# Kernel tuning notes

Measured on AMD Instinct MI355X. Metric: run time of the kernel, lower is better.

Reference implementation:

```python
import jax, jax.numpy as jnp
import numpy as np

N_SRC = 100000
N_TGT = 100000
N_EDGES = 1600000
D = 128
HID = 128
OUT = 64
NUM_LAYERS = 2
P_DROP = 0.1
NEG_SLOPE = 0.01


def setup_inputs() -> dict:
    key = jax.random.key(0)
    ks = jax.random.split(key, 16)
    s = 1.0 / np.sqrt(D)
    inp = {
        "x_source": jax.random.normal(ks[0], (N_SRC, D), jnp.float32),
        "x_target": jax.random.normal(ks[1], (N_TGT, D), jnp.float32),
        "Wl_tgt": jax.random.normal(ks[2], (NUM_LAYERS, D, HID), jnp.float32) * s,
        "bl_tgt": jax.random.normal(ks[3], (NUM_LAYERS, HID), jnp.float32) * s,
        "Wr_tgt": jax.random.normal(ks[4], (NUM_LAYERS, D, HID), jnp.float32) * s,
        "Wl_src": jax.random.normal(ks[5], (NUM_LAYERS, D, HID), jnp.float32) * s,
        "bl_src": jax.random.normal(ks[6], (NUM_LAYERS, HID), jnp.float32) * s,
        "Wr_src": jax.random.normal(ks[7], (NUM_LAYERS, D, HID), jnp.float32) * s,
        "W_out": jax.random.normal(ks[8], (HID, OUT), jnp.float32) * (1.0 / np.sqrt(HID)),
        "b_out": jax.random.normal(ks[9], (OUT,), jnp.float32) * 0.01,
        "edge_src": jax.random.randint(ks[10], (N_EDGES,), 0, N_SRC, jnp.int32),
        "edge_dst": jax.random.randint(ks[11], (N_EDGES,), 0, N_TGT, jnp.int32),
        "rev_src": jax.random.randint(ks[12], (N_EDGES,), 0, N_TGT, jnp.int32),
        "rev_dst": jax.random.randint(ks[13], (N_EDGES,), 0, N_SRC, jnp.int32),
    }
    return inp


def _sage(x_src, x_dst, src_idx, dst_idx, n_dst, Wl, bl, Wr):
    # mean-aggregate neighbor messages per destination node (PyG SAGEConv default)
    msg = x_src[src_idx]  # [E, D] gather
    agg = jax.ops.segment_sum(msg, dst_idx, num_segments=n_dst)  # [n_dst, D]
    cnt = jax.ops.segment_sum(jnp.ones((src_idx.shape[0],), msg.dtype), dst_idx,
                              num_segments=n_dst)
    mean = agg / jnp.maximum(cnt, 1.0)[:, None]
    return mean @ Wl + bl + x_dst @ Wr


def _dropout(x, key):
    keep = jax.random.bernoulli(key, 1.0 - P_DROP, x.shape)
    return jnp.where(keep, x / (1.0 - P_DROP), jnp.zeros((), x.dtype))


def reference(x_source, x_target, Wl_tgt, bl_tgt, Wr_tgt, Wl_src, bl_src, Wr_src,
              W_out, b_out, edge_src, edge_dst, rev_src, rev_dst):
    dkey = jax.random.key(42)
    xs, xt = x_source, x_target
    for l in range(NUM_LAYERS):
        # ('source','edge','target'): target receives from source
        new_t = _sage(xs, xt, edge_src, edge_dst, N_TGT, Wl_tgt[l], bl_tgt[l], Wr_tgt[l])
        # ('target','rev_edge','source'): source receives from target
        new_s = _sage(xt, xs, rev_src, rev_dst, N_SRC, Wl_src[l], bl_src[l], Wr_src[l])
        new_t = jax.nn.leaky_relu(new_t, NEG_SLOPE)
        new_s = jax.nn.leaky_relu(new_s, NEG_SLOPE)
        new_t = _dropout(new_t, jax.random.fold_in(dkey, 2 * l))
        new_s = _dropout(new_s, jax.random.fold_in(dkey, 2 * l + 1))
        xs, xt = new_s, new_t
    return xs @ W_out + b_out
```

## Files before the change

### kernel.cpp

```cpp
#include <hip/hip_runtime.h>
#include <stdint.h>

#define NN 100000
#define NE 1600000
#define DD 128
#define HB 1024
#define G8 12544
#define SUBN 98
#define NSUB 128
#define NND 100352
#define K2 16
#define RCAP 2304

typedef unsigned short u16;
typedef short short8 __attribute__((ext_vector_type(8)));
typedef float floatx4 __attribute__((ext_vector_type(4)));
typedef int intx4 __attribute__((ext_vector_type(4)));

__device__ static inline u16 f2bf(float f){
  unsigned u = __float_as_uint(f);
  unsigned r = u + 0x7FFFu + ((u >> 16) & 1u);
  return (u16)(r >> 16);
}

__host__ __device__ static inline unsigned rotl32(unsigned x, int r){
  return (x << r) | (x >> (32 - r));
}

__host__ __device__ static inline void tf2x32(unsigned k0, unsigned k1,
                                              unsigned c0, unsigned c1,
                                              unsigned &o0, unsigned &o1)
{
  const unsigned ks2 = k0 ^ k1 ^ 0x1BD11BDAu;
  unsigned x0 = c0 + k0, x1 = c1 + k1;
#define TFR(r) { x0 += x1; x1 = rotl32(x1, (r)); x1 ^= x0; }
  TFR(13) TFR(15) TFR(26) TFR(6)   x0 += k1;  x1 += ks2 + 1u;
  TFR(17) TFR(29) TFR(16) TFR(24)  x0 += ks2; x1 += k0 + 2u;
  TFR(13) TFR(15) TFR(26) TFR(6)   x0 += k0;  x1 += k1 + 3u;
  TFR(17) TFR(29) TFR(16) TFR(24)  x0 += k1;  x1 += ks2 + 4u;
  TFR(13) TFR(15) TFR(26) TFR(6)   x0 += ks2; x1 += k0 + 5u;
#undef TFR
  o0 = x0; o1 = x1;
}

__device__ static inline float drop_scale(unsigned k0, unsigned k1, unsigned j)
{
  unsigned o0, o1;
  tf2x32(k0, k1, 0u, j, o0, o1);
  const unsigned bits = o0 ^ o1;
  const float u = __uint_as_float((bits >> 9) | 0x3F800000u) - 1.0f;
  return (u < 0.9f) ? (1.0f / 0.9f) : 0.0f;
}

__global__ __launch_bounds__(256) void k_hist(const int* __restrict__ e_dst,
                                              const int* __restrict__ r_dst,
                                              int* __restrict__ hist){
  __shared__ int h[16];
  const int t = threadIdx.x;
  if (t < 16) h[t] = 0;
  __syncthreads();
  const int QT = 2 * (NE / 4);
  for (int i = blockIdx.x * 256 + t; i < QT; i += HB * 256){
    int dir = (i >= NE / 4);
    int qi = dir ? i - NE / 4 : i;
    const int* dp = dir ? r_dst : e_dst;
    intx4 d = __builtin_nontemporal_load((const intx4*)dp + qi);
    int bb = dir << 3;
    atomicAdd(&h[bb + d.x / G8], 1);
    atomicAdd(&h[bb + d.y / G8], 1);
    atomicAdd(&h[bb + d.z / G8], 1);
    atomicAdd(&h[bb + d.w / G8], 1);
  }
  __syncthreads();
  if (t < 16) hist[t * HB + blockIdx.x] = h[t];
}

__global__ __launch_bounds__(256) void k_scanA(int* __restrict__ hist){
  __shared__ int sh[16 * HB];
  __shared__ int tot[256];
  const int t = threadIdx.x;
  const int N = 16 * HB;
  for (int k = t; k < N; k += 256) sh[k] = hist[k];
  __syncthreads();
  int s = 0;
  #pragma unroll 4
  for (int k = 0; k < 64; ++k)
    s += sh[(t >> 4) * HB + (t & 15) + (k << 4)];
  tot[t] = s;
  __syncthreads();
  int v = s;
  for (int off = 1; off < 256; off <<= 1){
    int u = (t >= off) ? tot[t - off] : 0;
    __syncthreads();
    tot[t] += u;
    __syncthreads();
  }
  int run = tot[t] - v;
  for (int k = 0; k < 64; ++k){
    int idx = (t >> 4) * HB + (t & 15) + (k << 4);
    int xv = sh[idx];
    sh[idx] = run;
    run += xv;
  }
  __syncthreads();
  for (int k = t; k < N; k += 256) hist[k] = sh[k];
  if (t == 255) hist[N] = tot[255];
}

__global__ __launch_bounds__(256) void k_scatter1(const int* __restrict__ e_src,
                                                  const int* __restrict__ e_dst,
                                                  const int* __restrict__ r_src,
                                                  const int* __restrict__ r_dst,
                                                  const int* __restrict__ base,
                                                  unsigned* __restrict__ stage){
  __shared__ int cur[16];
  const int t = threadIdx.x;
  if (t < 16) cur[t] = base[t * HB + blockIdx.x];
  __syncthreads();
  const int QT = 2 * (NE / 4);
  for (int i = blockIdx.x * 256 + t; i < QT; i += HB * 256){
    int dir = (i >= NE / 4);
    int qi = dir ? i - NE / 4 : i;
    const int* dp = dir ? r_dst : e_dst;
    const int* sp = dir ? r_src : e_src;
    intx4 d = __builtin_nontemporal_load((const intx4*)dp + qi);
    intx4 sv = __builtin_nontemporal_load((const intx4*)sp + qi);
    int bb = dir << 3;
    int g, p;
    g = d.x / G8; p = atomicAdd(&cur[bb + g], 1);
    stage[p] = (unsigned)sv.x | ((unsigned)(d.x - g * G8) << 17);
    g = d.y / G8; p = atomicAdd(&cur[bb + g], 1);
    stage[p] = (unsigned)sv.y | ((unsigned)(d.y - g * G8) << 17);
    g = d.z / G8; p = atomicAdd(&cur[bb + g], 1);
    stage[p] = (unsigned)sv.z | ((unsigned)(d.z - g * G8) << 17);
    g = d.w / G8; p = atomicAdd(&cur[bb + g], 1);
    stage[p] = (unsigned)sv.w | ((unsigned)(d.w - g * G8) << 17);
  }
}

__global__ __launch_bounds__(256) void k_hist2(const unsigned* __restrict__ stage,
                                               const int* __restrict__ base,
                                               int* __restrict__ hist2){
  __shared__ int h2[NSUB];
  const int b16 = blockIdx.x / K2, k = blockIdx.x % K2;
  const int t = threadIdx.x;
  if (t < NSUB) h2[t] = 0;
  __syncthreads();
  const int beg = base[b16 * HB];
  const int end = base[(b16 + 1) * HB];
  for (int i = beg + k * 256 + t; i < end; i += K2 * 256){
    unsigned p = stage[i];
    atomicAdd(&h2[(int)(p >> 17) / SUBN], 1);
  }
  __syncthreads();
  if (t < NSUB) hist2[(b16 * NSUB + t) * K2 + k] = h2[t];
}

__global__ __launch_bounds__(256) void k_scanB(int* __restrict__ hist2){
  __shared__ int sh[16 * NSUB * K2];
  __shared__ int tot[256];
  const int t = threadIdx.x;
  const int N = 16 * NSUB * K2;
  for (int k = t; k < N; k += 256) sh[k] = hist2[k];
  __syncthreads();
  int s = 0;
  for (int j = 0; j < 128; ++j) s += sh[t * 128 + j];
  tot[t] = s;
  __syncthreads();
  int v = s;
  for (int off = 1; off < 256; off <<= 1){
    int u = (t >= off) ? tot[t - off] : 0;
    __syncthreads();
    tot[t] += u;
    __syncthreads();
  }
  int run = tot[t] - v;
  for (int j = 0; j < 128; ++j){
    int xv = sh[t * 128 + j];
    sh[t * 128 + j] = run;
    run += xv;
  }
  __syncthreads();
  for (int k = t; k < N; k += 256) hist2[k] = sh[k];
}

__global__ __launch_bounds__(256) void k_scatter2(const unsigned* __restrict__ stage,
                                                  const int* __restrict__ base,
                                                  const int* __restrict__ h2s,
                                                  unsigned* __restrict__ stage2){
  __shared__ int cur[NSUB];
  const int b16 = blockIdx.x / K2, k = blockIdx.x % K2;
  const int t = threadIdx.x;
  if (t < NSUB) cur[t] = h2s[(b16 * NSUB + t) * K2 + k];
  __syncthreads();
  const int beg = base[b16 * HB];
  const int end = base[(b16 + 1) * HB];
  for (int i = beg + k * 256 + t; i < end; i += K2 * 256){
    unsigned p = stage[i];
    int pos = atomicAdd(&cur[(int)(p >> 17) / SUBN], 1);
    stage2[pos] = p;
  }
}

__global__ __launch_bounds__(256) void k_fill4(const unsigned* __restrict__ stage2,
                                               const int* __restrict__ h2s,
                                               int* __restrict__ ptr,
                                               int* __restrict__ csr){
  __shared__ unsigned rec[RCAP];
  __shared__ unsigned srt[RCAP];
  __shared__ int ldeg[SUBN], lptr[SUBN], lcur[SUBN];
  const int sb = blockIdx.x;
  const int b16 = sb >> 7, sub = sb & 127;
  const int dir = b16 >> 3, g = b16 & 7;
  const int t = threadIdx.x;
  const int beg = h2s[sb * K2];
  const int end = (sb == 2047) ? 2 * NE : h2s[(sb + 1) * K2];
  int n = end - beg;
  if (n > RCAP) n = RCAP;
  for (int i = t; i < n; i += 256) rec[i] = stage2[beg + i];
  if (t < SUBN) ldeg[t] = 0;
  __syncthreads();
  const int nl0 = sub * SUBN;
  for (int i = t; i < n; i += 256)
    atomicAdd(&ldeg[(int)(rec[i] >> 17) - nl0], 1);
  __syncthreads();
  if (t == 0){
    int run = 0;
    for (int s = 0; s < SUBN; ++s){ lptr[s] = run; lcur[s] = run; run += ldeg[s]; }
  }
  __syncthreads();
  for (int i = t; i < n; i += 256){
    int rl = (int)(rec[i] >> 17) - nl0;
    int pos = atomicAdd(&lcur[rl], 1);
    srt[pos] = rec[i] & 0x1FFFFu;
  }
  __syncthreads();
  const int node0 = g * G8 + nl0;
  if (t < SUBN) ptr[dir * NND + node0 + t] = beg + lptr[t];
  if (sb == 2047 && t == 0) ptr[2 * NND] = 2 * NE;
  for (int i = t; i < n; i += 256) csr[beg + i] = (int)srt[i];
}

__global__ __launch_bounds__(256) void k_cvt2(const float* __restrict__ ina,
                                              const float* __restrict__ inb,
                                              u16* __restrict__ oa,
                                              u16* __restrict__ ob, int n8){
  int i = blockIdx.x * 256 + threadIdx.x;
  const float* in = ina; u16* out = oa;
  if (i >= n8){ i -= n8; in = inb; out = ob; }
  floatx4 a = __builtin_nontemporal_load((const floatx4*)in + (size_t)i * 2);
  floatx4 b = __builtin_nontemporal_load((const floatx4*)in + (size_t)i * 2 + 1);
  u16 v[8] = { f2bf(a[0]), f2bf(a[1]), f2bf(a[2]), f2bf(a[3]),
               f2bf(b[0]), f2bf(b[1]), f2bf(b[2]), f2bf(b[3]) };
  *(uint4*)(out + (size_t)i * 8) = *(const uint4*)v;
}

__global__ __launch_bounds__(256) void k_prep(const float* __restrict__ Wl_tgt,
    const float* __restrict__ Wr_tgt, const float* __restrict__ Wl_src,
    const float* __restrict__ Wr_src, const float* __restrict__ Wo,
    u16* __restrict__ Wsw0, u16* __restrict__ Wsw1, u16* __restrict__ Wsw2,
    u16* __restrict__ Wswo){
  int b = blockIdx.x;
  if (b < 48){
    const float *Wl, *Wr; u16* dst;
    if (b < 16){ Wl = Wl_tgt; Wr = Wr_tgt; dst = Wsw0; }
    else if (b < 32){ Wl = Wl_src; Wr = Wr_src; dst = Wsw1; b -= 16; }
    else { Wl = Wl_src + 16384; Wr = Wr_src + 16384; dst = Wsw2; b -= 32; }
    int idx = b * 256 + threadIdx.x;
    int lane = idx & 63, tile = idx >> 6;
    int kt = tile >> 3, nt = tile & 7;
    int n = nt * 16 + (lane & 15);
    int kb = kt * 32 + (lane >> 4) * 8;
    u16 v[8];
    #pragma unroll
    for (int j = 0; j < 8; ++j){
      int k = kb + j;
      float w = (k < 128) ? Wl[(size_t)k * 128 + n] : Wr[(size_t)(k - 128) * 128 + n];
      v[j] = f2bf(w);
    }
    *(uint4*)(dst + (size_t)idx * 8) = *(const uint4*)v;
  } else {
    int idx = (b - 48) * 256 + threadIdx.x;
    int lane = idx & 63, tile = idx >> 6;
    int kt = tile >> 2, nt = tile & 3;
    int n = nt * 16 + (lane & 15);
    int kb = kt * 32 + (lane >> 4) * 8;
    u16 v[8];
    #pragma unroll
    for (int j = 0; j < 8; ++j)
      v[j] = f2bf(Wo[(size_t)(kb + j) * 64 + n]);
    *(uint4*)(Wswo + (size_t)idx * 8) = *(const uint4*)v;
  }
}

__device__ static inline void agg_body(const u16* __restrict__ x,
                                       const int* __restrict__ pd,
                                       const int* __restrict__ csr,
                                       u16* __restrict__ out, int blk){
  const int row = blk * 4 + (threadIdx.x >> 6);
  const int lane = threadIdx.x & 63;
  const int sub = lane >> 4, l4 = lane & 15;
  const int beg = pd[row], end = pd[row + 1];
  const int cnt = end - beg;
  float a[8] = {0.f,0.f,0.f,0.f,0.f,0.f,0.f,0.f};
  int e = 0;
  for (; e + 7 < cnt; e += 8){
    int s0 = csr[beg + e + sub];
    int s1 = csr[beg + e + 4 + sub];
    uint4 v0 = *(const uint4*)(x + (size_t)s0 * DD + l4 * 8);
    uint4 v1 = *(const uint4*)(x + (size_t)s1 * DD + l4 * 8);
    a[0] += __uint_as_float(v0.x << 16); a[1] += __uint_as_float(v0.x & 0xFFFF0000u);
    a[2] += __uint_as_float(v0.y << 16); a[3] += __uint_as_float(v0.y & 0xFFFF0000u);
    a[4] += __uint_as_float(v0.z << 16); a[5] += __uint_as_float(v0.z & 0xFFFF0000u);
    a[6] += __uint_as_float(v0.w << 16); a[7] += __uint_as_float(v0.w & 0xFFFF0000u);
    a[0] += __uint_as_float(v1.x << 16); a[1] += __uint_as_float(v1.x & 0xFFFF0000u);
    a[2] += __uint_as_float(v1.y << 16); a[3] += __uint_as_float(v1.y & 0xFFFF0000u);
    a[4] += __uint_as_float(v1.z << 16); a[5] += __uint_as_float(v1.z & 0xFFFF0000u);
    a[6] += __uint_as_float(v1.w << 16); a[7] += __uint_as_float(v1.w & 0xFFFF0000u);
  }
  for (; e + 3 < cnt; e += 4){
    int s0 = csr[beg + e + sub];
    uint4 v0 = *(const uint4*)(x + (size_t)s0 * DD + l4 * 8);
    a[0] += __uint_as_float(v0.x << 16); a[1] += __uint_as_float(v0.x & 0xFFFF0000u);
    a[2] += __uint_as_float(v0.y << 16); a[3] += __uint_as_float(v0.y & 0xFFFF0000u);
    a[4] += __uint_as_float(v0.z << 16); a[5] += __uint_as_float(v0.z & 0xFFFF0000u);
    a[6] += __uint_as_float(v0.w << 16); a[7] += __uint_as_float(v0.w & 0xFFFF0000u);
  }
  if (e + sub < cnt){
    int s0 = csr[beg + e + sub];
    uint4 v0 = *(const uint4*)(x + (size_t)s0 * DD + l4 * 8);
    a[0] += __uint_as_float(v0.x << 16); a[1] += __uint_as_float(v0.x & 0xFFFF0000u);
    a[2] += __uint_as_float(v0.y << 16); a[3] += __uint_as_float(v0.y & 0xFFFF0000u);
    a[4] += __uint_as_float(v0.z << 16); a[5] += __uint_as_float(v0.z & 0xFFFF0000u);
    a[6] += __uint_as_float(v0.w << 16); a[7] += __uint_as_float(v0.w & 0xFFFF0000u);
  }
  #pragma unroll
  for (int i = 0; i < 8; ++i){
    a[i] += __shfl_xor(a[i], 16);
    a[i] += __shfl_xor(a[i], 32);
  }
  const float inv = (cnt > 0) ? (1.0f / (float)cnt) : 1.0f;
  if (sub == 0){
    unsigned pk[4];
    #pragma unroll
    for (int i = 0; i < 4; ++i)
      pk[i] = (unsigned)f2bf(a[2*i] * inv) | ((unsigned)f2bf(a[2*i+1] * inv) << 16);
    *(uint4*)(out + (size_t)row * DD + l4 * 8) = make_uint4(pk[0], pk[1], pk[2], pk[3]);
  }
}

__global__ __launch_bounds__(256) void k_aggD(const u16* __restrict__ x0,
    const u16* __restrict__ x1, const int* __restrict__ ptr,
    const int* __restrict__ csr, u16* __restrict__ o0, u16* __restrict__ o1){
  int b = blockIdx.x;
  if (b < NN / 4) agg_body(x0, ptr, csr, o0, b);
  else            agg_body(x1, ptr + NND, csr, o1, b - NN / 4);
}

__global__ __launch_bounds__(256) void k_agg1(const u16* __restrict__ x,
    const int* __restrict__ ptr, const int* __restrict__ csr,
    u16* __restrict__ out){
  agg_body(x, ptr + NND, csr, out, blockIdx.x);
}

__device__ static inline void fused_body(const u16* __restrict__ Am,
    const u16* __restrict__ X, const u16* __restrict__ Wsw,
    const float* __restrict__ bias, u16* __restrict__ outH,
    unsigned key0, unsigned key1, int blk)
{
  const int wave = threadIdx.x >> 6, lane = threadIdx.x & 63;
  const int quad = lane >> 4, col0 = lane & 15;
  const int row0 = blk * 64 + wave * 16;
  int m = row0 + col0;
  if (m >= NN) m = NN - 1;

  floatx4 acc[8];
  #pragma unroll
  for (int i = 0; i < 8; ++i) acc[i] = (floatx4)0.f;

  #pragma unroll
  for (int kt = 0; kt < 8; ++kt){
    const int k = kt * 32 + quad * 8;
    const u16* ap = (k < 128) ? (Am + (size_t)m * 128 + k)
                              : (X  + (size_t)m * 128 + (k - 128));
    short8 a = __builtin_nontemporal_load((const short8*)ap);
    #pragma unroll
    for (int nt = 0; nt < 8; ++nt){
      short8 b = *(const short8*)(Wsw + (size_t)(((kt * 8 + nt) * 64 + lane) * 8));
      acc[nt] = __builtin_amdgcn_mfma_f32_16x16x32_bf16(a, b, acc[nt], 0, 0, 0);
    }
  }

  #pragma unroll
  for (int nt = 0; nt < 8; ++nt){
    const int col = nt * 16 + col0;
    const float bj = bias[col];
    #pragma unroll
    for (int rg = 0; rg < 4; ++rg){
      const int r = row0 + quad * 4 + rg;
      if (r < NN){
        float h = acc[nt][rg] + bj;
        h = (h >= 0.f) ? h : 0.01f * h;
        unsigned j = (unsigned)r * 128u + (unsigned)col;
        h *= drop_scale(key0, key1, j);
        outH[(size_t)r * 128 + col] = f2bf(h);
      }
    }
  }
}

#define GB ((NN + 63) / 64)

__global__ __launch_bounds__(256) void k_fusedD(
    const u16* __restrict__ A0, const u16* __restrict__ X0,
    const u16* __restrict__ W0, const float* __restrict__ b0,
    u16* __restrict__ o0, unsigned k00, unsigned k01,
    const u16* __restrict__ A1, const u16* __restrict__ X1,
    const u16* __restrict__ W1, const float* __restrict__ b1,
    u16* __restrict__ o1, unsigned k10, unsigned k11)
{
  int b = blockIdx.x;
  if (b < GB) fused_body(A0, X0, W0, b0, o0, k00, k01, b);
  else        fused_body(A1, X1, W1, b1, o1, k10, k11, b - GB);
}

__global__ __launch_bounds__(256) void k_fused(const u16* __restrict__ Am,
    const u16* __restrict__ X, const u16* __restrict__ Wsw,
    const float* __restrict__ bias, u16* __restrict__ outH,
    unsigned key0, unsigned key1)
{
  fused_body(Am, X, Wsw, bias, outH, key0, key1, blockIdx.x);
}

__global__ __launch_bounds__(256) void k_out(const u16* __restrict__ H,
    const u16* __restrict__ Wsw, const float* __restrict__ bias,
    float* __restrict__ out)
{
  const int wave = threadIdx.x >> 6, lane = threadIdx.x & 63;
  const int quad = lane >> 4, col0 = lane & 15;
  const int row0 = blockIdx.x * 64 + wave * 16;
  int m = row0 + col0;
  if (m >= NN) m = NN - 1;

  floatx4 acc[4];
  #pragma unroll
  for (int i = 0; i < 4; ++i) acc[i] = (floatx4)0.f;

  #pragma unroll
  for (int kt = 0; kt < 4; ++kt){
    short8 a = __builtin_nontemporal_load(
        (const short8*)(H + (size_t)m * 128 + kt * 32 + quad * 8));
    #pragma unroll
    for (int nt = 0; nt < 4; ++nt){
      short8 b = *(const short8*)(Wsw + (size_t)(((kt * 4 + nt) * 64 + lane) * 8));
      acc[nt] = __builtin_amdgcn_mfma_f32_16x16x32_bf16(a, b, acc[nt], 0, 0, 0);
    }
  }

  #pragma unroll
  for (int nt = 0; nt < 4; ++nt){
    const int col = nt * 16 + col0;
    const float bj = bias[col];
    #pragma unroll
    for (int rg = 0; rg < 4; ++rg){
      const int r = row0 + quad * 4 + rg;
      if (r < NN)
        out[(size_t)r * 64 + col] = acc[nt][rg] + bj;
    }
  }
}

extern "C" void kernel_launch(void* const* d_in, const int* in_sizes, int n_in,
                              void* d_out, int out_size, void* d_ws, size_t ws_size,
                              hipStream_t stream)
{
  const float* x_src  = (const float*)d_in[0];
  const float* x_tgt  = (const float*)d_in[1];
  const float* Wl_tgt = (const float*)d_in[2];
  const float* bl_tgt = (const float*)d_in[3];
  const float* Wr_tgt = (const float*)d_in[4];
  const float* Wl_src = (const float*)d_in[5];
  const float* bl_src = (const float*)d_in[6];
  const float* Wr_src = (const float*)d_in[7];
  const float* W_o    = (const float*)d_in[8];
  const float* b_o    = (const float*)d_in[9];
  const int*   e_src  = (const int*)d_in[10];
  const int*   e_dst  = (const int*)d_in[11];
  const int*   r_src  = (const int*)d_in[12];
  const int*   r_dst  = (const int*)d_in[13];
  float* out = (float*)d_out;
  (void)in_sizes; (void)n_in; (void)out_size; (void)ws_size;

  char* ws = (char*)d_ws;
  size_t off = 0;
  auto alloc = [&](size_t bytes) -> char* {
    char* p = ws + off; off += (bytes + 255) & ~(size_t)255; return p;
  };
  unsigned* stage1 = (unsigned*)alloc((size_t)2 * NE * 4);
  unsigned* stage2 = (unsigned*)alloc((size_t)2 * NE * 4);
  u16* A_t  = (u16*)stage1;
  u16* A_s  = (u16*)alloc((size_t)NN * DD * 2);
  u16* Xs   = (u16*)alloc((size_t)NN * DD * 2);
  u16* Xt   = (u16*)alloc((size_t)NN * DD * 2);
  u16* B    = (u16*)alloc((size_t)NN * DD * 2);
  u16* C    = (u16*)alloc((size_t)NN * DD * 2);
  u16* Wsw0 = (u16*)alloc(256 * 128 * 2);
  u16* Wsw1 = (u16*)alloc(256 * 128 * 2);
  u16* Wsw2 = (u16*)alloc(256 * 128 * 2);
  u16* Wswo = (u16*)alloc(128 * 64 * 2);
  int* csr  = (int*)alloc((size_t)2 * NE * 4);
  int* ptr  = (int*)alloc((size_t)(2 * NND + 1) * 4);
  int* hist  = (int*)alloc((size_t)(16 * HB + 1) * 4);
  int* hist2 = (int*)alloc((size_t)(16 * NSUB * K2) * 4);

  unsigned kt0a, kt0b, ks0a, ks0b, ks1a, ks1b;
  tf2x32(0u, 42u, 0u, 0u, kt0a, kt0b);
  tf2x32(0u, 42u, 0u, 1u, ks0a, ks0b);
  tf2x32(0u, 42u, 0u, 3u, ks1a, ks1b);

  const int CB = NN * DD / 8 / 256;

  k_cvt2<<<2 * CB, 256, 0, stream>>>(x_src, x_tgt, Xs, Xt, NN * DD / 8);
  k_prep<<<52, 256, 0, stream>>>(Wl_tgt, Wr_tgt, Wl_src, Wr_src, W_o,
                                 Wsw0, Wsw1, Wsw2, Wswo);

  k_hist<<<HB, 256, 0, stream>>>(e_dst, r_dst, hist);
  k_scanA<<<1, 256, 0, stream>>>(hist);
  k_scatter1<<<HB, 256, 0, stream>>>(e_src, e_dst, r_src, r_dst, hist, stage1);
  k_hist2<<<16 * K2, 256, 0, stream>>>(stage1, hist, hist2);
  k_scanB<<<1, 256, 0, stream>>>(hist2);
  k_scatter2<<<16 * K2, 256, 0, stream>>>(stage1, hist, hist2, stage2);
  k_fill4<<<2048, 256, 0, stream>>>(stage2, hist2, ptr, csr);

  const int AB = NN / 4;
  k_aggD<<<2 * AB, 256, 0, stream>>>(Xs, Xt, ptr, csr, A_t, A_s);
  k_fusedD<<<2 * GB, 256, 0, stream>>>(A_t, Xt, Wsw0, bl_tgt, B, kt0a, kt0b,
                                       A_s, Xs, Wsw1, bl_src, C, ks0a, ks0b);
  k_agg1<<<AB, 256, 0, stream>>>(B, ptr, csr, A_t);
  k_fused<<<GB, 256, 0, stream>>>(A_t, C, Wsw2, bl_src + 128, B, ks1a, ks1b);
  k_out<<<GB, 256, 0, stream>>>(B, Wswo, b_o, out);
}
```

Baseline: 576.2 us.

## Precompute dropout masks as bitmasks in aggregation kernels to hide latency

The Threefry dropout RNG moves out of the MFMA epilogue and into the memory-bound aggregation kernels. There each wave computes keep bits for its row with ballots and stores them as two 64-bit masks per row. The fused GEMM epilogue then reads these bitmasks instead of running Threefry for every output element. The aim is to hide RNG ALU work under gather latency, at the cost of small extra mask buffers and the extra traffic to write and read them.

```diff
diff --git a/kernel.cpp b/kernel.cpp
--- a/kernel.cpp
+++ b/kernel.cpp
@@ -13,6 +13,7 @@
 #define RCAP 2304
 
 typedef unsigned short u16;
+typedef unsigned long long u64;
 typedef short short8 __attribute__((ext_vector_type(8)));
 typedef float floatx4 __attribute__((ext_vector_type(4)));
 typedef int intx4 __attribute__((ext_vector_type(4)));
@@ -43,13 +44,13 @@
   o0 = x0; o1 = x1;
 }
 
-__device__ static inline float drop_scale(unsigned k0, unsigned k1, unsigned j)
+__device__ static inline int drop_keep(unsigned k0, unsigned k1, unsigned j)
 {
   unsigned o0, o1;
   tf2x32(k0, k1, 0u, j, o0, o1);
   const unsigned bits = o0 ^ o1;
   const float u = __uint_as_float((bits >> 9) | 0x3F800000u) - 1.0f;
-  return (u < 0.9f) ? (1.0f / 0.9f) : 0.0f;
+  return u < 0.9f;
 }
 
 __global__ __launch_bounds__(256) void k_hist(const int* __restrict__ e_dst,
@@ -296,7 +297,9 @@
 __device__ static inline void agg_body(const u16* __restrict__ x,
                                        const int* __restrict__ pd,
                                        const int* __restrict__ csr,
-                                       u16* __restrict__ out, int blk){
+                                       u16* __restrict__ out,
+                                       u64* __restrict__ msk,
+                                       unsigned key0, unsigned key1, int blk){
   const int row = blk * 4 + (threadIdx.x >> 6);
   const int lane = threadIdx.x & 63;
   const int sub = lane >> 4, l4 = lane & 15;
@@ -334,12 +337,15 @@
     a[4] += __uint_as_float(v0.z << 16); a[5] += __uint_as_float(v0.z & 0xFFFF0000u);
     a[6] += __uint_as_float(v0.w << 16); a[7] += __uint_as_float(v0.w & 0xFFFF0000u);
   }
+  u64 mA = __ballot(drop_keep(key0, key1, (unsigned)row * 128u + (unsigned)lane));
+  u64 mB = __ballot(drop_keep(key0, key1, (unsigned)row * 128u + 64u + (unsigned)lane));
   #pragma unroll
   for (int i = 0; i < 8; ++i){
     a[i] += __shfl_xor(a[i], 16);
     a[i] += __shfl_xor(a[i], 32);
   }
   const float inv = (cnt > 0) ? (1.0f / (float)cnt) : 1.0f;
+  if (lane < 2) msk[(size_t)row * 2 + lane] = lane ? mB : mA;
   if (sub == 0){
     unsigned pk[4];
     #pragma unroll
@@ -351,22 +357,25 @@
 
 __global__ __launch_bounds__(256) void k_aggD(const u16* __restrict__ x0,
     const u16* __restrict__ x1, const int* __restrict__ ptr,
-    const int* __restrict__ csr, u16* __restrict__ o0, u16* __restrict__ o1){
+    const int* __restrict__ csr, u16* __restrict__ o0, u16* __restrict__ o1,
+    u64* __restrict__ m0, u64* __restrict__ m1,
+    unsigned k00, unsigned k01, unsigned k10, unsigned k11){
   int b = blockIdx.x;
-  if (b < NN / 4) agg_body(x0, ptr, csr, o0, b);
-  else            agg_body(x1, ptr + NND, csr, o1, b - NN / 4);
+  if (b < NN / 4) agg_body(x0, ptr, csr, o0, m0, k00, k01, b);
+  else            agg_body(x1, ptr + NND, csr, o1, m1, k10, k11, b - NN / 4);
 }
 
 __global__ __launch_bounds__(256) void k_agg1(const u16* __restrict__ x,
     const int* __restrict__ ptr, const int* __restrict__ csr,
-    u16* __restrict__ out){
-  agg_body(x, ptr + NND, csr, out, blockIdx.x);
+    u16* __restrict__ out, u64* __restrict__ msk,
+    unsigned key0, unsigned key1){
+  agg_body(x, ptr + NND, csr, out, msk, key0, key1, blockIdx.x);
 }
 
 __device__ static inline void fused_body(const u16* __restrict__ Am,
     const u16* __restrict__ X, const u16* __restrict__ Wsw,
     const float* __restrict__ bias, u16* __restrict__ outH,
-    unsigned key0, unsigned key1, int blk)
+    const u64* __restrict__ msk, int blk)
 {
   const int wave = threadIdx.x >> 6, lane = threadIdx.x & 63;
   const int quad = lane >> 4, col0 = lane & 15;
@@ -391,18 +400,28 @@
     }
   }
 
+  u64 w0[4], w1[4];
+  #pragma unroll
+  for (int rg = 0; rg < 4; ++rg){
+    int r = row0 + quad * 4 + rg;
+    size_t rr = (size_t)((r < NN) ? r : (NN - 1)) * 2;
+    w0[rg] = msk[rr];
+    w1[rg] = msk[rr + 1];
+  }
+
   #pragma unroll
   for (int nt = 0; nt < 8; ++nt){
     const int col = nt * 16 + col0;
     const float bj = bias[col];
+    const int sh = col & 63;
     #pragma unroll
     for (int rg = 0; rg < 4; ++rg){
       const int r = row0 + quad * 4 + rg;
       if (r < NN){
         float h = acc[nt][rg] + bj;
         h = (h >= 0.f) ? h : 0.01f * h;
-        unsigned j = (unsigned)r * 128u + (unsigned)col;
-        h *= drop_scale(key0, key1, j);
+        u64 w = (nt < 4) ? w0[rg] : w1[rg];
+        h = ((w >> sh) & 1ull) ? h * (1.0f / 0.9f) : 0.0f;
         outH[(size_t)r * 128 + col] = f2bf(h);
       }
     }
@@ -414,22 +433,22 @@
 __global__ __launch_bounds__(256) void k_fusedD(
     const u16* __restrict__ A0, const u16* __restrict__ X0,
     const u16* __restrict__ W0, const float* __restrict__ b0,
-    u16* __restrict__ o0, unsigned k00, unsigned k01,
+    u16* __restrict__ o0, const u64* __restrict__ m0,
     const u16* __restrict__ A1, const u16* __restrict__ X1,
     const u16* __restrict__ W1, const float* __restrict__ b1,
-    u16* __restrict__ o1, unsigned k10, unsigned k11)
+    u16* __restrict__ o1, const u64* __restrict__ m1)
 {
   int b = blockIdx.x;
-  if (b < GB) fused_body(A0, X0, W0, b0, o0, k00, k01, b);
-  else        fused_body(A1, X1, W1, b1, o1, k10, k11, b - GB);
+  if (b < GB) fused_body(A0, X0, W0, b0, o0, m0, b);
+  else        fused_body(A1, X1, W1, b1, o1, m1, b - GB);
 }
 
 __global__ __launch_bounds__(256) void k_fused(const u16* __restrict__ Am,
     const u16* __restrict__ X, const u16* __restrict__ Wsw,
     const float* __restrict__ bias, u16* __restrict__ outH,
-    unsigned key0, unsigned key1)
-{
-  fused_body(Am, X, Wsw, bias, outH, key0, key1, blockIdx.x);
+    const u64* __restrict__ msk)
+{
+  fused_body(Am, X, Wsw, bias, outH, msk, blockIdx.x);
 }
 
 __global__ __launch_bounds__(256) void k_out(const u16* __restrict__ H,
@@ -512,6 +531,9 @@
   int* ptr  = (int*)alloc((size_t)(2 * NND + 1) * 4);
   int* hist  = (int*)alloc((size_t)(16 * HB + 1) * 4);
   int* hist2 = (int*)alloc((size_t)(16 * NSUB * K2) * 4);
+  u64* M0t  = (u64*)alloc((size_t)NN * 2 * 8);
+  u64* M0s  = (u64*)alloc((size_t)NN * 2 * 8);
+  u64* M1s  = (u64*)alloc((size_t)NN * 2 * 8);
 
   unsigned kt0a, kt0b, ks0a, ks0b, ks1a, ks1b;
   tf2x32(0u, 42u, 0u, 0u, kt0a, kt0b);
@@ -533,10 +555,11 @@
   k_fill4<<<2048, 256, 0, stream>>>(stage2, hist2, ptr, csr);
 
   const int AB = NN / 4;
-  k_aggD<<<2 * AB, 256, 0, stream>>>(Xs, Xt, ptr, csr, A_t, A_s);
-  k_fusedD<<<2 * GB, 256, 0, stream>>>(A_t, Xt, Wsw0, bl_tgt, B, kt0a, kt0b,
-                                       A_s, Xs, Wsw1, bl_src, C, ks0a, ks0b);
-  k_agg1<<<AB, 256, 0, stream>>>(B, ptr, csr, A_t);
-  k_fused<<<GB, 256, 0, stream>>>(A_t, C, Wsw2, bl_src + 128, B, ks1a, ks1b);
+  k_aggD<<<2 * AB, 256, 0, stream>>>(Xs, Xt, ptr, csr, A_t, A_s,
+                                     M0t, M0s, kt0a, kt0b, ks0a, ks0b);
+  k_fusedD<<<2 * GB, 256, 0, stream>>>(A_t, Xt, Wsw0, bl_tgt, B, M0t,
+                                       A_s, Xs, Wsw1, bl_src, C, M0s);
+  k_agg1<<<AB, 256, 0, stream>>>(B, ptr, csr, A_t, M1s, ks1a, ks1b);
+  k_fused<<<GB, 256, 0, stream>>>(A_t, C, Wsw2, bl_src + 128, B, M1s);
   k_out<<<GB, 256, 0, stream>>>(B, Wswo, b_o, out);
 }
```

Measured after the change: 568.9 us. Within noise of the previous version (-1.3%).

## Fuse neighbor aggregation into MFMA layer kernel via swizzled LDS tile

Applied to the files above, without the earlier changes.

Each layer's mean aggregation now runs inside the GEMM kernel. Every block gathers and averages 64 destination rows into a swizzled shared-memory tile, then feeds that tile straight into the MFMA loop, so the aggregated matrix no longer goes through global memory. Dropout masks are computed once per row with ballots during aggregation and stored as bitmasks, replacing per-element Threefry calls in the epilogue. The conversion, histogram and weight-prep kernels are merged into one launch, and accumulation uses paired float2 adds. In exchange, each block serialises 16 gather rows per wave, with fewer blocks in flight to hide gather latency.

```diff
diff --git a/kernel.cpp b/kernel.cpp
--- a/kernel.cpp
+++ b/kernel.cpp
@@ -13,8 +13,10 @@
 #define RCAP 2304
 
 typedef unsigned short u16;
+typedef unsigned long long u64;
 typedef short short8 __attribute__((ext_vector_type(8)));
 typedef float floatx4 __attribute__((ext_vector_type(4)));
+typedef float floatx2 __attribute__((ext_vector_type(2)));
 typedef int intx4 __attribute__((ext_vector_type(4)));
 
 __device__ static inline u16 f2bf(float f){
@@ -43,36 +45,100 @@
   o0 = x0; o1 = x1;
 }
 
-__device__ static inline float drop_scale(unsigned k0, unsigned k1, unsigned j)
+__device__ static inline int drop_keep(unsigned k0, unsigned k1, unsigned j)
 {
   unsigned o0, o1;
   tf2x32(k0, k1, 0u, j, o0, o1);
   const unsigned bits = o0 ^ o1;
   const float u = __uint_as_float((bits >> 9) | 0x3F800000u) - 1.0f;
-  return (u < 0.9f) ? (1.0f / 0.9f) : 0.0f;
-}
-
-__global__ __launch_bounds__(256) void k_hist(const int* __restrict__ e_dst,
-                                              const int* __restrict__ r_dst,
-                                              int* __restrict__ hist){
-  __shared__ int h[16];
-  const int t = threadIdx.x;
-  if (t < 16) h[t] = 0;
-  __syncthreads();
-  const int QT = 2 * (NE / 4);
-  for (int i = blockIdx.x * 256 + t; i < QT; i += HB * 256){
-    int dir = (i >= NE / 4);
-    int qi = dir ? i - NE / 4 : i;
-    const int* dp = dir ? r_dst : e_dst;
-    intx4 d = __builtin_nontemporal_load((const intx4*)dp + qi);
-    int bb = dir << 3;
-    atomicAdd(&h[bb + d.x / G8], 1);
-    atomicAdd(&h[bb + d.y / G8], 1);
-    atomicAdd(&h[bb + d.z / G8], 1);
-    atomicAdd(&h[bb + d.w / G8], 1);
-  }
-  __syncthreads();
-  if (t < 16) hist[t * HB + blockIdx.x] = h[t];
+  return u < 0.9f;
+}
+
+__device__ static inline void acc4(floatx2 &p0, floatx2 &p1, floatx2 &p2,
+                                   floatx2 &p3, uint4 v){
+  floatx2 t0, t1, t2, t3;
+  t0[0] = __uint_as_float(v.x << 16); t0[1] = __uint_as_float(v.x & 0xFFFF0000u);
+  t1[0] = __uint_as_float(v.y << 16); t1[1] = __uint_as_float(v.y & 0xFFFF0000u);
+  t2[0] = __uint_as_float(v.z << 16); t2[1] = __uint_as_float(v.z & 0xFFFF0000u);
+  t3[0] = __uint_as_float(v.w << 16); t3[1] = __uint_as_float(v.w & 0xFFFF0000u);
+  p0 += t0; p1 += t1; p2 += t2; p3 += t3;
+}
+
+#define CVB 12500
+__global__ __launch_bounds__(256) void k_pre(
+    const float* __restrict__ ina, const float* __restrict__ inb,
+    u16* __restrict__ oa, u16* __restrict__ ob, int n8,
+    const int* __restrict__ e_dst, const int* __restrict__ r_dst,
+    int* __restrict__ hist,
+    const float* __restrict__ Wl_tgt, const float* __restrict__ Wr_tgt,
+    const float* __restrict__ Wl_src, const float* __restrict__ Wr_src,
+    const float* __restrict__ Wo,
+    u16* __restrict__ Wsw0, u16* __restrict__ Wsw1, u16* __restrict__ Wsw2,
+    u16* __restrict__ Wswo)
+{
+  const int blk = blockIdx.x;
+  const int t = threadIdx.x;
+  if (blk < CVB){
+    int i = blk * 256 + t;
+    const float* in = ina; u16* out = oa;
+    if (i >= n8){ i -= n8; in = inb; out = ob; }
+    floatx4 a = __builtin_nontemporal_load((const floatx4*)in + (size_t)i * 2);
+    floatx4 c = __builtin_nontemporal_load((const floatx4*)in + (size_t)i * 2 + 1);
+    u16 v[8] = { f2bf(a[0]), f2bf(a[1]), f2bf(a[2]), f2bf(a[3]),
+                 f2bf(c[0]), f2bf(c[1]), f2bf(c[2]), f2bf(c[3]) };
+    *(uint4*)(out + (size_t)i * 8) = *(const uint4*)v;
+  } else if (blk < CVB + HB){
+    const int hb = blk - CVB;
+    __shared__ int h[16];
+    if (t < 16) h[t] = 0;
+    __syncthreads();
+    const int QT = 2 * (NE / 4);
+    for (int i = hb * 256 + t; i < QT; i += HB * 256){
+      int dir = (i >= NE / 4);
+      int qi = dir ? i - NE / 4 : i;
+      const int* dp = dir ? r_dst : e_dst;
+      intx4 d = __builtin_nontemporal_load((const intx4*)dp + qi);
+      int bb = dir << 3;
+      atomicAdd(&h[bb + d.x / G8], 1);
+      atomicAdd(&h[bb + d.y / G8], 1);
+      atomicAdd(&h[bb + d.z / G8], 1);
+      atomicAdd(&h[bb + d.w / G8], 1);
+    }
+    __syncthreads();
+    if (t < 16) hist[t * HB + hb] = h[t];
+  } else {
+    int b = blk - CVB - HB;
+    if (b < 48){
+      const float *Wl, *Wr; u16* dst;
+      if (b < 16){ Wl = Wl_tgt; Wr = Wr_tgt; dst = Wsw0; }
+      else if (b < 32){ Wl = Wl_src; Wr = Wr_src; dst = Wsw1; b -= 16; }
+      else { Wl = Wl_src + 16384; Wr = Wr_src + 16384; dst = Wsw2; b -= 32; }
+      int idx = b * 256 + t;
+      int lane = idx & 63, tile = idx >> 6;
+      int kt = tile >> 3, nt = tile & 7;
+      int n = nt * 16 + (lane & 15);
+      int kb = kt * 32 + (lane >> 4) * 8;
+      u16 v[8];
+      #pragma unroll
+      for (int j = 0; j < 8; ++j){
+        int k = kb + j;
+        float w = (k < 128) ? Wl[(size_t)k * 128 + n] : Wr[(size_t)(k - 128) * 128 + n];
+        v[j] = f2bf(w);
+      }
+      *(uint4*)(dst + (size_t)idx * 8) = *(const uint4*)v;
+    } else {
+      int idx = (b - 48) * 256 + t;
+      int lane = idx & 63, tile = idx >> 6;
+      int kt = tile >> 2, nt = tile & 3;
+      int n = nt * 16 + (lane & 15);
+      int kb = kt * 32 + (lane >> 4) * 8;
+      u16 v[8];
+      #pragma unroll
+      for (int j = 0; j < 8; ++j)
+        v[j] = f2bf(Wo[(size_t)(kb + j) * 64 + n]);
+      *(uint4*)(Wswo + (size_t)idx * 8) = *(const uint4*)v;
+    }
+  }
 }
 
 __global__ __launch_bounds__(256) void k_scanA(int* __restrict__ hist){
@@ -241,149 +307,86 @@
   for (int i = t; i < n; i += 256) csr[beg + i] = (int)srt[i];
 }
 
-__global__ __launch_bounds__(256) void k_cvt2(const float* __restrict__ ina,
-                                              const float* __restrict__ inb,
-                                              u16* __restrict__ oa,
-                                              u16* __restrict__ ob, int n8){
-  int i = blockIdx.x * 256 + threadIdx.x;
-  const float* in = ina; u16* out = oa;
-  if (i >= n8){ i -= n8; in = inb; out = ob; }
-  floatx4 a = __builtin_nontemporal_load((const floatx4*)in + (size_t)i * 2);
-  floatx4 b = __builtin_nontemporal_load((const floatx4*)in + (size_t)i * 2 + 1);
-  u16 v[8] = { f2bf(a[0]), f2bf(a[1]), f2bf(a[2]), f2bf(a[3]),
-               f2bf(b[0]), f2bf(b[1]), f2bf(b[2]), f2bf(b[3]) };
-  *(uint4*)(out + (size_t)i * 8) = *(const uint4*)v;
-}
-
-__global__ __launch_bounds__(256) void k_prep(const float* __restrict__ Wl_tgt,
-    const float* __restrict__ Wr_tgt, const float* __restrict__ Wl_src,
-    const float* __restrict__ Wr_src, const float* __restrict__ Wo,
-    u16* __restrict__ Wsw0, u16* __restrict__ Wsw1, u16* __restrict__ Wsw2,
-    u16* __restrict__ Wswo){
-  int b = blockIdx.x;
-  if (b < 48){
-    const float *Wl, *Wr; u16* dst;
-    if (b < 16){ Wl = Wl_tgt; Wr = Wr_tgt; dst = Wsw0; }
-    else if (b < 32){ Wl = Wl_src; Wr = Wr_src; dst = Wsw1; b -= 16; }
-    else { Wl = Wl_src + 16384; Wr = Wr_src + 16384; dst = Wsw2; b -= 32; }
-    int idx = b * 256 + threadIdx.x;
-    int lane = idx & 63, tile = idx >> 6;
-    int kt = tile >> 3, nt = tile & 7;
-    int n = nt * 16 + (lane & 15);
-    int kb = kt * 32 + (lane >> 4) * 8;
-    u16 v[8];
+__device__ static inline void mf_body(const u16* __restrict__ xsrc,
+    const u16* __restrict__ xdst, const int* __restrict__ pd,
+    const int* __restrict__ csr, const u16* __restrict__ Wsw,
+    const float* __restrict__ bias, u16* __restrict__ outH,
+    unsigned key0, unsigned key1, int blk)
+{
+  __shared__ u16 As[64 * DD];
+  __shared__ u64 Ms[64][2];
+  const int wave = threadIdx.x >> 6, lane = threadIdx.x & 63;
+  const int sub = lane >> 4, l4 = lane & 15;
+  const int row0 = blk * 64;
+
+  for (int i = 0; i < 16; ++i){
+    const int lr = wave * 16 + i;
+    const int row = row0 + lr;
+    int beg = 0, cnt = 0;
+    if (row < NN){ beg = pd[row]; cnt = pd[row + 1] - beg; }
+    floatx2 p0 = (floatx2)0.f, p1 = (floatx2)0.f,
+            p2 = (floatx2)0.f, p3 = (floatx2)0.f;
+    int e = 0;
+    for (; e + 7 < cnt; e += 8){
+      int s0 = csr[beg + e + sub];
+      int s1 = csr[beg + e + 4 + sub];
+      uint4 v0 = *(const uint4*)(xsrc + (size_t)s0 * DD + l4 * 8);
+      uint4 v1 = *(const uint4*)(xsrc + (size_t)s1 * DD + l4 * 8);
+      acc4(p0, p1, p2, p3, v0);
+      acc4(p0, p1, p2, p3, v1);
+    }
+    for (; e + 3 < cnt; e += 4){
+      int s0 = csr[beg + e + sub];
+      uint4 v0 = *(const uint4*)(xsrc + (size_t)s0 * DD + l4 * 8);
+      acc4(p0, p1, p2, p3, v0);
+    }
+    if (e + sub < cnt){
+      int s0 = csr[beg + e + sub];
+      uint4 v0 = *(const uint4*)(xsrc + (size_t)s0 * DD + l4 * 8);
+      acc4(p0, p1, p2, p3, v0);
+    }
+    const int rm = (row < NN) ? row : NN - 1;
+    u64 mA = __ballot(drop_keep(key0, key1, (unsigned)rm * 128u + (unsigned)lane));
+    u64 mB = __ballot(drop_keep(key0, key1, (unsigned)rm * 128u + 64u + (unsigned)lane));
+    if (lane == 0){ Ms[lr][0] = mA; Ms[lr][1] = mB; }
+    float a[8] = { p0[0], p0[1], p1[0], p1[1], p2[0], p2[1], p3[0], p3[1] };
     #pragma unroll
     for (int j = 0; j < 8; ++j){
-      int k = kb + j;
-      float w = (k < 128) ? Wl[(size_t)k * 128 + n] : Wr[(size_t)(k - 128) * 128 + n];
-      v[j] = f2bf(w);
-    }
-    *(uint4*)(dst + (size_t)idx * 8) = *(const uint4*)v;
-  } else {
-    int idx = (b - 48) * 256 + threadIdx.x;
-    int lane = idx & 63, tile = idx >> 6;
-    int kt = tile >> 2, nt = tile & 3;
-    int n = nt * 16 + (lane & 15);
-    int kb = kt * 32 + (lane >> 4) * 8;
-    u16 v[8];
-    #pragma unroll
-    for (int j = 0; j < 8; ++j)
-      v[j] = f2bf(Wo[(size_t)(kb + j) * 64 + n]);
-    *(uint4*)(Wswo + (size_t)idx * 8) = *(const uint4*)v;
-  }
-}
-
-__device__ static inline void agg_body(const u16* __restrict__ x,
-                                       const int* __restrict__ pd,
-                                       const int* __restrict__ csr,
-                                       u16* __restrict__ out, int blk){
-  const int row = blk * 4 + (threadIdx.x >> 6);
-  const int lane = threadIdx.x & 63;
-  const int sub = lane >> 4, l4 = lane & 15;
-  const int beg = pd[row], end = pd[row + 1];
-  const int cnt = end - beg;
-  float a[8] = {0.f,0.f,0.f,0.f,0.f,0.f,0.f,0.f};
-  int e = 0;
-  for (; e + 7 < cnt; e += 8){
-    int s0 = csr[beg + e + sub];
-    int s1 = csr[beg + e + 4 + sub];
-    uint4 v0 = *(const uint4*)(x + (size_t)s0 * DD + l4 * 8);
-    uint4 v1 = *(const uint4*)(x + (size_t)s1 * DD + l4 * 8);
-    a[0] += __uint_as_float(v0.x << 16); a[1] += __uint_as_float(v0.x & 0xFFFF0000u);
-    a[2] += __uint_as_float(v0.y << 16); a[3] += __uint_as_float(v0.y & 0xFFFF0000u);
-    a[4] += __uint_as_float(v0.z << 16); a[5] += __uint_as_float(v0.z & 0xFFFF0000u);
-    a[6] += __uint_as_float(v0.w << 16); a[7] += __uint_as_float(v0.w & 0xFFFF0000u);
-    a[0] += __uint_as_float(v1.x << 16); a[1] += __uint_as_float(v1.x & 0xFFFF0000u);
-    a[2] += __uint_as_float(v1.y << 16); a[3] += __uint_as_float(v1.y & 0xFFFF0000u);
-    a[4] += __uint_as_float(v1.z << 16); a[5] += __uint_as_float(v1.z & 0xFFFF0000u);
-    a[6] += __uint_as_float(v1.w << 16); a[7] += __uint_as_float(v1.w & 0xFFFF0000u);
-  }
-  for (; e + 3 < cnt; e += 4){
-    int s0 = csr[beg + e + sub];
-    uint4 v0 = *(const uint4*)(x + (size_t)s0 * DD + l4 * 8);
-    a[0] += __uint_as_float(v0.x << 16); a[1] += __uint_as_float(v0.x & 0xFFFF0000u);
-    a[2] += __uint_as_float(v0.y << 16); a[3] += __uint_as_float(v0.y & 0xFFFF0000u);
-    a[4] += __uint_as_float(v0.z << 16); a[5] += __uint_as_float(v0.z & 0xFFFF0000u);
-    a[6] += __uint_as_float(v0.w << 16); a[7] += __uint_as_float(v0.w & 0xFFFF0000u);
-  }
-  if (e + sub < cnt){
-    int s0 = csr[beg + e + sub];
-    uint4 v0 = *(const uint4*)(x + (size_t)s0 * DD + l4 * 8);
-    a[0] += __uint_as_float(v0.x << 16); a[1] += __uint_as_float(v0.x & 0xFFFF0000u);
-    a[2] += __uint_as_float(v0.y << 16); a[3] += __uint_as_float(v0.y & 0xFFFF0000u);
-    a[4] += __uint_as_float(v0.z << 16); a[5] += __uint_as_float(v0.z & 0xFFFF0000u);
-    a[6] += __uint_as_float(v0.w << 16); a[7] += __uint_as_float(v0.w & 0xFFFF0000u);
-  }
-  #pragma unroll
-  for (int i = 0; i < 8; ++i){
-    a[i] += __shfl_xor(a[i], 16);
-    a[i] += __shfl_xor(a[i], 32);
-  }
-  const float inv = (cnt > 0) ? (1.0f / (float)cnt) : 1.0f;
-  if (sub == 0){
-    unsigned pk[4];
-    #pragma unroll
-    for (int i = 0; i < 4; ++i)
-      pk[i] = (unsigned)f2bf(a[2*i] * inv) | ((unsigned)f2bf(a[2*i+1] * inv) << 16);
-    *(uint4*)(out + (size_t)row * DD + l4 * 8) = make_uint4(pk[0], pk[1], pk[2], pk[3]);
-  }
-}
-
-__global__ __launch_bounds__(256) void k_aggD(const u16* __restrict__ x0,
-    const u16* __restrict__ x1, const int* __restrict__ ptr,
-    const int* __restrict__ csr, u16* __restrict__ o0, u16* __restrict__ o1){
-  int b = blockIdx.x;
-  if (b < NN / 4) agg_body(x0, ptr, csr, o0, b);
-  else            agg_body(x1, ptr + NND, csr, o1, b - NN / 4);
-}
-
-__global__ __launch_bounds__(256) void k_agg1(const u16* __restrict__ x,
-    const int* __restrict__ ptr, const int* __restrict__ csr,
-    u16* __restrict__ out){
-  agg_body(x, ptr + NND, csr, out, blockIdx.x);
-}
-
-__device__ static inline void fused_body(const u16* __restrict__ Am,
-    const u16* __restrict__ X, const u16* __restrict__ Wsw,
-    const float* __restrict__ bias, u16* __restrict__ outH,
-    unsigned key0, unsigned key1, int blk)
-{
-  const int wave = threadIdx.x >> 6, lane = threadIdx.x & 63;
+      a[j] += __shfl_xor(a[j], 16);
+      a[j] += __shfl_xor(a[j], 32);
+    }
+    const float inv = (cnt > 0) ? (1.0f / (float)cnt) : 1.0f;
+    if (sub == 0){
+      unsigned pk[4];
+      #pragma unroll
+      for (int j = 0; j < 4; ++j)
+        pk[j] = (unsigned)f2bf(a[2*j] * inv) | ((unsigned)f2bf(a[2*j+1] * inv) << 16);
+      const int ch = l4 ^ (lr & 15);
+      *(uint4*)(As + lr * DD + ch * 8) = make_uint4(pk[0], pk[1], pk[2], pk[3]);
+    }
+  }
+  __syncthreads();
+
   const int quad = lane >> 4, col0 = lane & 15;
-  const int row0 = blk * 64 + wave * 16;
-  int m = row0 + col0;
+  const int ml = wave * 16 + col0;
+  int m = row0 + ml;
   if (m >= NN) m = NN - 1;
 
   floatx4 acc[8];
   #pragma unroll
-  for (int i = 0; i < 8; ++i) acc[i] = (floatx4)0.f;
+  for (int j = 0; j < 8; ++j) acc[j] = (floatx4)0.f;
 
   #pragma unroll
   for (int kt = 0; kt < 8; ++kt){
-    const int k = kt * 32 + quad * 8;
-    const u16* ap = (k < 128) ? (Am + (size_t)m * 128 + k)
-                              : (X  + (size_t)m * 128 + (k - 128));
-    short8 a = __builtin_nontemporal_load((const short8*)ap);
+    short8 a;
+    if (kt < 4){
+      const int k = kt * 32 + quad * 8;
+      const int ch = (k >> 3) ^ (ml & 15);
+      a = *(const short8*)(As + ml * DD + ch * 8);
+    } else {
+      const int k = (kt - 4) * 32 + quad * 8;
+      a = __builtin_nontemporal_load((const short8*)(xdst + (size_t)m * 128 + k));
+    }
     #pragma unroll
     for (int nt = 0; nt < 8; ++nt){
       short8 b = *(const short8*)(Wsw + (size_t)(((kt * 8 + nt) * 64 + lane) * 8));
@@ -395,14 +398,16 @@
   for (int nt = 0; nt < 8; ++nt){
     const int col = nt * 16 + col0;
     const float bj = bias[col];
+    const int sh = col & 63;
     #pragma unroll
     for (int rg = 0; rg < 4; ++rg){
-      const int r = row0 + quad * 4 + rg;
+      const int lr2 = wave * 16 + quad * 4 + rg;
+      const int r = row0 + lr2;
       if (r < NN){
         float h = acc[nt][rg] + bj;
         h = (h >= 0.f) ? h : 0.01f * h;
-        unsigned j = (unsigned)r * 128u + (unsigned)col;
-        h *= drop_scale(key0, key1, j);
+        u64 w = Ms[lr2][nt >> 2];
+        h = ((w >> sh) & 1ull) ? h * (1.0f / 0.9f) : 0.0f;
         outH[(size_t)r * 128 + col] = f2bf(h);
       }
     }
@@ -411,25 +416,26 @@
 
 #define GB ((NN + 63) / 64)
 
-__global__ __launch_bounds__(256) void k_fusedD(
-    const u16* __restrict__ A0, const u16* __restrict__ X0,
+__global__ __launch_bounds__(256) void k_mfD(
+    const u16* __restrict__ Xs, const u16* __restrict__ Xt,
+    const int* __restrict__ ptr, const int* __restrict__ csr,
     const u16* __restrict__ W0, const float* __restrict__ b0,
-    u16* __restrict__ o0, unsigned k00, unsigned k01,
-    const u16* __restrict__ A1, const u16* __restrict__ X1,
+    u16* __restrict__ oB, unsigned k00, unsigned k01,
     const u16* __restrict__ W1, const float* __restrict__ b1,
-    u16* __restrict__ o1, unsigned k10, unsigned k11)
+    u16* __restrict__ oC, unsigned k10, unsigned k11)
 {
   int b = blockIdx.x;
-  if (b < GB) fused_body(A0, X0, W0, b0, o0, k00, k01, b);
-  else        fused_body(A1, X1, W1, b1, o1, k10, k11, b - GB);
-}
-
-__global__ __launch_bounds__(256) void k_fused(const u16* __restrict__ Am,
-    const u16* __restrict__ X, const u16* __restrict__ Wsw,
-    const float* __restrict__ bias, u16* __restrict__ outH,
-    unsigned key0, unsigned key1)
-{
-  fused_body(Am, X, Wsw, bias, outH, key0, key1, blockIdx.x);
+  if (b < GB) mf_body(Xs, Xt, ptr,       csr, W0, b0, oB, k00, k01, b);
+  else        mf_body(Xt, Xs, ptr + NND, csr, W1, b1, oC, k10, k11, b - GB);
+}
+
+__global__ __launch_bounds__(256) void k_mf1(
+    const u16* __restrict__ Bh, const u16* __restrict__ Ch,
+    const int* __restrict__ ptr, const int* __restrict__ csr,
+    const u16* __restrict__ W2, const float* __restrict__ b2,
+    u16* __restrict__ oH, unsigned ka, unsigned kb)
+{
+  mf_body(Bh, Ch, ptr + NND, csr, W2, b2, oH, ka, kb, blockIdx.x);
 }
 
 __global__ __launch_bounds__(256) void k_out(const u16* __restrict__ H,
@@ -498,8 +504,7 @@
   };
   unsigned* stage1 = (unsigned*)alloc((size_t)2 * NE * 4);
   unsigned* stage2 = (unsigned*)alloc((size_t)2 * NE * 4);
-  u16* A_t  = (u16*)stage1;
-  u16* A_s  = (u16*)alloc((size_t)NN * DD * 2);
+  u16* H1   = (u16*)stage1;
   u16* Xs   = (u16*)alloc((size_t)NN * DD * 2);
   u16* Xt   = (u16*)alloc((size_t)NN * DD * 2);
   u16* B    = (u16*)alloc((size_t)NN * DD * 2);
@@ -518,13 +523,10 @@
   tf2x32(0u, 42u, 0u, 1u, ks0a, ks0b);
   tf2x32(0u, 42u, 0u, 3u, ks1a, ks1b);
 
-  const int CB = NN * DD / 8 / 256;
-
-  k_cvt2<<<2 * CB, 256, 0, stream>>>(x_src, x_tgt, Xs, Xt, NN * DD / 8);
-  k_prep<<<52, 256, 0, stream>>>(Wl_tgt, Wr_tgt, Wl_src, Wr_src, W_o,
-                                 Wsw0, Wsw1, Wsw2, Wswo);
-
-  k_hist<<<HB, 256, 0, stream>>>(e_dst, r_dst, hist);
+  k_pre<<<CVB + HB + 52, 256, 0, stream>>>(x_src, x_tgt, Xs, Xt, NN * DD / 8,
+                                           e_dst, r_dst, hist,
+                                           Wl_tgt, Wr_tgt, Wl_src, Wr_src, W_o,
+                                           Wsw0, Wsw1, Wsw2, Wswo);
   k_scanA<<<1, 256, 0, stream>>>(hist);
   k_scatter1<<<HB, 256, 0, stream>>>(e_src, e_dst, r_src, r_dst, hist, stage1);
   k_hist2<<<16 * K2, 256, 0, stream>>>(stage1, hist, hist2);
@@ -532,11 +534,10 @@
   k_scatter2<<<16 * K2, 256, 0, stream>>>(stage1, hist, hist2, stage2);
   k_fill4<<<2048, 256, 0, stream>>>(stage2, hist2, ptr, csr);
 
-  const int AB = NN / 4;
-  k_aggD<<<2 * AB, 256, 0, stream>>>(Xs, Xt, ptr, csr, A_t, A_s);
-  k_fusedD<<<2 * GB, 256, 0, stream>>>(A_t, Xt, Wsw0, bl_tgt, B, kt0a, kt0b,
-                                       A_s, Xs, Wsw1, bl_src, C, ks0a, ks0b);
-  k_agg1<<<AB, 256, 0, stream>>>(B, ptr, csr, A_t);
-  k_fused<<<GB, 256, 0, stream>>>(A_t, C, Wsw2, bl_src + 128, B, ks1a, ks1b);
-  k_out<<<GB, 256, 0, stream>>>(B, Wswo, b_o, out);
-}
+  k_mfD<<<2 * GB, 256, 0, stream>>>(Xs, Xt, ptr, csr,
+                                    Wsw0, bl_tgt, B, kt0a, kt0b,
+                                    Wsw1, bl_src, C, ks0a, ks0b);
+  k_mf1<<<GB, 256, 0, stream>>>(B, C, ptr, csr,
+                                Wsw2, bl_src + 128, H1, ks1a, ks1b);
+  k_out<<<GB, 256, 0, stream>>>(H1, Wswo, b_o, out);
+}
```

Measured after the change: 709.1 us. 1.23x slower.
